# Kernel tuning notes

Measured on AMD Instinct MI355X. Metric: run time of the kernel, lower is better.

Reference implementation:

```python
import jax, jax.numpy as jnp
import numpy as np

E = 1024   # embed_dim
H = 16     # num_heads
DH = E // H
FF = 4096  # intermediate_size
EPS = 1e-5


def layernorm(x, g, b):
    mu = jnp.mean(x, axis=-1, keepdims=True)
    var = jnp.var(x, axis=-1, keepdims=True)
    return (x - mu) * jax.lax.rsqrt(var + EPS) * g + b


def setup_inputs() -> dict:
    key = jax.random.key(0)
    ks = jax.random.split(key, 16)
    s = 0.02
    return {
        "x": jax.random.normal(ks[0], (2, 2048, E), dtype=jnp.float32),
        "ln1_g": jnp.ones((E,), jnp.float32),
        "ln1_b": jnp.zeros((E,), jnp.float32),
        "ln2_g": jnp.ones((E,), jnp.float32),
        "ln2_b": jnp.zeros((E,), jnp.float32),
        # per-head Q/K/V projections stacked: [H, E, DH]
        "wq": jax.random.normal(ks[1], (H, E, DH), jnp.float32) * s,
        "bq": jnp.zeros((H, DH), jnp.float32),
        "wk": jax.random.normal(ks[2], (H, E, DH), jnp.float32) * s,
        "bk": jnp.zeros((H, DH), jnp.float32),
        "wv": jax.random.normal(ks[3], (H, E, DH), jnp.float32) * s,
        "bv": jnp.zeros((H, DH), jnp.float32),
        "wo": jax.random.normal(ks[4], (E, E), jnp.float32) * s,
        "bo": jnp.zeros((E,), jnp.float32),
        "w1": jax.random.normal(ks[5], (E, FF), jnp.float32) * s,
        "b1": jnp.zeros((FF,), jnp.float32),
        "w2": jax.random.normal(ks[6], (FF, E), jnp.float32) * s,
        "b2": jnp.zeros((E,), jnp.float32),
    }


def reference(x, ln1_g, ln1_b, ln2_g, ln2_b, wq, bq, wk, bk, wv, bv,
              wo, bo, w1, b1, w2, b2):
    # --- multi-head attention (pre-LN) ---
    h = layernorm(x, ln1_g, ln1_b)                       # [B,S,E]
    q = jnp.einsum('bse,hed->bhsd', h, wq) + bq[:, None, :]
    k = jnp.einsum('bse,hed->bhsd', h, wk) + bk[:, None, :]
    v = jnp.einsum('bse,hed->bhsd', h, wv) + bv[:, None, :]
    scores = jnp.einsum('bhsd,bhtd->bhst', q, k) / jnp.sqrt(
        jnp.asarray(DH, x.dtype))                        # [B,H,S,S]
    w = jax.nn.softmax(scores, axis=-1)
    attn = jnp.einsum('bhst,bhtd->bhsd', w, v)           # [B,H,S,DH]
    B, _, S, _ = attn.shape
    concat = attn.transpose(0, 2, 1, 3).reshape(B, S, E)  # head concat order
    x = x + concat @ wo + bo
    # --- feed-forward (pre-LN), exact GELU, dropout_p=0 ---
    h2 = layernorm(x, ln2_g, ln2_b)
    ff = jax.nn.gelu(h2 @ w1 + b1, approximate=False) @ w2 + b2
    return x + ff
```

## Files before the change

kernel.cpp:

```cpp
#include <hip/hip_runtime.h>
#include <hip/hip_bf16.h>
#include <math.h>

typedef __attribute__((ext_vector_type(8))) short short8;
typedef __attribute__((ext_vector_type(4))) float f32x4;
typedef __attribute__((ext_vector_type(16))) float f32x16;
typedef __attribute__((ext_vector_type(4))) unsigned u32x4;

#define MFMA_BF16(a, b, c) __builtin_amdgcn_mfma_f32_16x16x32_bf16(a, b, c, 0, 0, 0)
#define MFMA32_BF16(a, b, c) __builtin_amdgcn_mfma_f32_32x32x16_bf16(a, b, c, 0, 0, 0)

#define GLD_LDS16(g, l)                                              \
  __builtin_amdgcn_global_load_lds(                                  \
      (const __attribute__((address_space(1))) void*)(g),            \
      (__attribute__((address_space(3))) void*)(l), 16, 0, 0)

__device__ __forceinline__ unsigned cvt_pk_bf16(float lo, float hi) {
  unsigned r;
  asm("v_cvt_pk_bf16_f32 %0, %1, %2" : "=v"(r) : "v"(lo), "v"(hi));
  return r;
}
#define PSWAP(a, b) asm volatile("v_permlane32_swap_b32 %0, %1" : "+v"(a), "+v"(b))

__device__ __forceinline__ unsigned short f2bf(float f) {
  union { float f; unsigned u; } v; v.f = f;
  unsigned r = v.u + 0x7FFFu + ((v.u >> 16) & 1u);
  return (unsigned short)(r >> 16);
}
__device__ __forceinline__ float bf2f(unsigned short u) {
  union { unsigned u; float f; } v; v.u = ((unsigned)u) << 16;
  return v.f;
}

__global__ __launch_bounds__(256) void transpose_cast(
    const float* __restrict__ in, unsigned short* __restrict__ out,
    int R, int C, size_t in_bs, size_t out_bs) {
  __shared__ float t[32][33];
  const float* inp = in + blockIdx.z * in_bs;
  unsigned short* outp = out + blockIdx.z * out_bs;
  const int c0 = blockIdx.x * 32, r0 = blockIdx.y * 32;
  const int tx = threadIdx.x, ty = threadIdx.y;
#pragma unroll
  for (int i = 0; i < 32; i += 8)
    t[ty + i][tx] = inp[(size_t)(r0 + ty + i) * C + c0 + tx];
  __syncthreads();
#pragma unroll
  for (int i = 0; i < 32; i += 8)
    outp[(size_t)(c0 + ty + i) * R + r0 + tx] = f2bf(t[tx][ty + i]);
}

__global__ void concat_bias(const float* __restrict__ bq, const float* __restrict__ bk,
                            const float* __restrict__ bv, float* __restrict__ bcat) {
  int i = blockIdx.x * 256 + threadIdx.x;
  if (i < 1024) bcat[i] = bq[i];
  else if (i < 2048) bcat[i] = bk[i - 1024];
  else if (i < 3072) bcat[i] = bv[i - 2048];
}

__global__ __launch_bounds__(512) void vtrans(
    const unsigned short* __restrict__ qkv, unsigned short* __restrict__ vt) {
  __shared__ unsigned short t[64][65];
  const int bh = blockIdx.y;
  const int s0 = blockIdx.x * 64;
  const int tx = threadIdx.x;
  const int ty = threadIdx.y;
  const unsigned short* in =
      qkv + (size_t)(bh >> 4) * 2048 * 3072 + 2048 + (bh & 15) * 64;
#pragma unroll
  for (int i = 0; i < 8; ++i)
    t[ty * 8 + i][tx] = in[(size_t)(s0 + ty * 8 + i) * 3072 + tx];
  __syncthreads();
  unsigned short* o = vt + (size_t)bh * 64 * 2048 + s0;
#pragma unroll
  for (int i = 0; i < 8; ++i)
    o[(size_t)(ty * 8 + i) * 2048 + tx] = t[tx][ty * 8 + i];
}

__global__ __launch_bounds__(256) void ln_kernel(
    const float* __restrict__ x, const float* __restrict__ g,
    const float* __restrict__ bb, unsigned short* __restrict__ out) {
  const int row = blockIdx.x, tid = threadIdx.x;
  const float4 v = ((const float4*)(x + (size_t)row * 1024))[tid];
  float s = v.x + v.y + v.z + v.w;
  float ss = v.x * v.x + v.y * v.y + v.z * v.z + v.w * v.w;
#pragma unroll
  for (int k = 1; k < 64; k <<= 1) {
    s += __shfl_xor(s, k, 64);
    ss += __shfl_xor(ss, k, 64);
  }
  __shared__ float red[8];
  const int wid = tid >> 6;
  if ((tid & 63) == 0) { red[wid] = s; red[wid + 4] = ss; }
  __syncthreads();
  s = red[0] + red[1] + red[2] + red[3];
  ss = red[4] + red[5] + red[6] + red[7];
  const float mu = s * (1.0f / 1024.0f);
  const float var = ss * (1.0f / 1024.0f) - mu * mu;
  const float rs = rsqrtf(var + 1e-5f);
  const float4 gv = ((const float4*)g)[tid];
  const float4 bv = ((const float4*)bb)[tid];
  ushort4 o;
  o.x = f2bf((v.x - mu) * rs * gv.x + bv.x);
  o.y = f2bf((v.y - mu) * rs * gv.y + bv.y);
  o.z = f2bf((v.z - mu) * rs * gv.z + bv.z);
  o.w = f2bf((v.w - mu) * rs * gv.w + bv.w);
  ((ushort4*)(out + (size_t)row * 1024))[tid] = o;
}

template <int EPI, int BN>
__global__ __launch_bounds__(256, 3) void gemm_bt(
    const unsigned short* __restrict__ A, const unsigned short* __restrict__ Bt,
    const float* __restrict__ bias, const float* __restrict__ res,
    void* __restrict__ Cout, int M, int N, int K) {
  constexpr int NFR = BN / 32;
  constexpr int BISS = BN / 32;
  __shared__ unsigned short As[128 * 64];
  __shared__ unsigned short Bs[BN * 64];
  const int tid = threadIdx.x;
  const int wid = tid >> 6, lane = tid & 63;
  const int li = lane & 15, gi = lane >> 4;
  const int bm = blockIdx.y, bn = blockIdx.x;
  const int wr = (wid >> 1) << 6;
  const int wc = (wid & 1) * (BN / 2);

  f32x4 acc[4][NFR];
#pragma unroll
  for (int m = 0; m < 4; ++m)
#pragma unroll
    for (int n = 0; n < NFR; ++n) acc[m][n] = (f32x4)0.0f;

  const size_t Ksz = (size_t)K;
  const int srow = tid >> 3;
  const int segG = (tid & 7) ^ (srow & 7);
  const unsigned short* Ab = A + (size_t)(bm * 128 + srow) * Ksz + segG * 8;
  const unsigned short* Bb = Bt + (size_t)(bn * BN + srow) * Ksz + segG * 8;

  for (int kt = 0; kt < K; kt += 64) {
#pragma unroll
    for (int c = 0; c < 4; ++c)
      GLD_LDS16(Ab + (size_t)(c * 32) * Ksz + kt, As + c * 2048 + wid * 512);
#pragma unroll
    for (int c = 0; c < BISS; ++c)
      GLD_LDS16(Bb + (size_t)(c * 32) * Ksz + kt, Bs + c * 2048 + wid * 512);
    __syncthreads();
    short8 af[4][2], bf[NFR][2];
#pragma unroll
    for (int m = 0; m < 4; ++m)
#pragma unroll
      for (int kk = 0; kk < 2; ++kk) {
        const int row = wr + m * 16 + li;
        af[m][kk] = *(const short8*)(As + row * 64 + ((kk * 4 + gi) ^ (row & 7)) * 8);
      }
#pragma unroll
    for (int n = 0; n < NFR; ++n)
#pragma unroll
      for (int kk = 0; kk < 2; ++kk) {
        const int row = wc + n * 16 + li;
        bf[n][kk] = *(const short8*)(Bs + row * 64 + ((kk * 4 + gi) ^ (row & 7)) * 8);
      }
    __builtin_amdgcn_s_setprio(1);
#pragma unroll
    for (int m = 0; m < 4; ++m)
#pragma unroll
      for (int n = 0; n < NFR; ++n) {
        acc[m][n] = MFMA_BF16(af[m][0], bf[n][0], acc[m][n]);
        acc[m][n] = MFMA_BF16(af[m][1], bf[n][1], acc[m][n]);
      }
    __builtin_amdgcn_s_setprio(0);
    __syncthreads();
  }

  const int row_base = bm * 128 + wr + gi * 4;
  const int col_base = bn * BN + wc + li;
#pragma unroll
  for (int m = 0; m < 4; ++m) {
#pragma unroll
    for (int n = 0; n < NFR; ++n) {
      const int col = col_base + n * 16;
      const float bi = bias[col];
#pragma unroll
      for (int r = 0; r < 4; ++r) {
        const int row = row_base + m * 16 + r;
        float v = acc[m][n][r] + bi;
        if (EPI == 2) v = 0.5f * v * (1.0f + erff(v * 0.70710678118654752f));
        const size_t idx = (size_t)row * N + col;
        if (EPI == 1) ((float*)Cout)[idx] = v + res[idx];
        else ((unsigned short*)Cout)[idx] = f2bf(v);
      }
    }
  }
}

__global__ __launch_bounds__(256, 4) void attn_kernel(
    const unsigned short* __restrict__ qkv, const unsigned short* __restrict__ vt,
    unsigned short* __restrict__ op0, unsigned short* __restrict__ op1,
    float* __restrict__ lpart) {
  __shared__ unsigned short Kl[2][4096];
  const int tid = threadIdx.x;
  const int wid = tid >> 6, lane = tid & 63;
  const int l31 = lane & 31, hiq = lane >> 5;
  const int kvh = blockIdx.z & 1, b = blockIdx.z >> 1, h = blockIdx.y;
  const int q0 = blockIdx.x * 128 + wid * 32;
  const int LD = 3072;
  const size_t base = (size_t)b * 2048 * LD;
  const size_t kvoff = (size_t)kvh * 1024 * LD;

  short8 qb[4];
  {
    const unsigned short* qp = qkv + base + (size_t)(q0 + l31) * LD + h * 64 + hiq * 8;
#pragma unroll
    for (int ds = 0; ds < 4; ++ds) qb[ds] = *(const short8*)(qp + ds * 16);
  }

  f32x16 o0 = (f32x16)0.0f, o1 = (f32x16)0.0f;
  float la = 0.0f, lb = 0.0f;

  const int krw = lane >> 3;
  const int ksegG = (lane & 7) ^ krw;
  const unsigned short* kdma = qkv + base + kvoff + 1024 + h * 64 + ksegG * 8 +
                               (size_t)(wid * 16 + krw) * LD;

  const unsigned short* vbh =
      vt + (size_t)(b * 16 + h) * 64 * 2048 + kvh * 1024 + 8 * hiq;

  auto kstage = [&](int buf, int t) {
    GLD_LDS16(kdma + (size_t)t * 64 * LD, &Kl[buf][wid * 1024]);
    GLD_LDS16(kdma + (size_t)(t * 64 + 8) * LD, &Kl[buf][wid * 1024 + 512]);
  };

  kstage(0, 0);
  __syncthreads();

  for (int t = 0; t < 16; ++t) {
    if (t < 15) kstage((t + 1) & 1, t + 1);

    const unsigned short* kl = Kl[t & 1];
    short8 kf[2][4];
#pragma unroll
    for (int kvb = 0; kvb < 2; ++kvb)
#pragma unroll
      for (int ds = 0; ds < 4; ++ds)
        kf[kvb][ds] = *(const short8*)(
            kl + (kvb * 32 + l31) * 64 + (((2 * ds + hiq) ^ (l31 & 7)) * 8));

    f32x16 sA = (f32x16)0.0f, sB = (f32x16)0.0f;
    __builtin_amdgcn_s_setprio(1);
#pragma unroll
    for (int ds = 0; ds < 4; ++ds) {
      sA = MFMA32_BF16(kf[0][ds], qb[ds], sA);
      sB = MFMA32_BF16(kf[1][ds], qb[ds], sB);
    }
    __builtin_amdgcn_s_setprio(0);

    const unsigned short* vtt = vbh + 64 * t;
#pragma unroll
    for (int kvb = 0; kvb < 2; ++kvb) {
      const int ks0 = 2 * kvb;
      const short8 v00 = *(const short8*)(vtt + (size_t)l31 * 2048 + 16 * ks0);
      const short8 v01 = *(const short8*)(vtt + (size_t)l31 * 2048 + 16 * ks0 + 16);
      const short8 v10 = *(const short8*)(vtt + (size_t)(32 + l31) * 2048 + 16 * ks0);
      const short8 v11 = *(const short8*)(vtt + (size_t)(32 + l31) * 2048 + 16 * ks0 + 16);
      const f32x16 s = kvb ? sB : sA;
      unsigned P[8];
#pragma unroll
      for (int i = 0; i < 8; ++i) {
        const float pe = __expf(s[2 * i] * 0.125f);
        const float po = __expf(s[2 * i + 1] * 0.125f);
        la += pe; lb += po;
        P[i] = cvt_pk_bf16(pe, po);
      }
      PSWAP(P[0], P[2]); PSWAP(P[1], P[3]);
      PSWAP(P[4], P[6]); PSWAP(P[5], P[7]);
      const short8 pa0 = __builtin_bit_cast(short8, (u32x4){P[0], P[1], P[2], P[3]});
      const short8 pa1 = __builtin_bit_cast(short8, (u32x4){P[4], P[5], P[6], P[7]});
      __builtin_amdgcn_s_setprio(1);
      o0 = MFMA32_BF16(pa0, v00, o0);
      o0 = MFMA32_BF16(pa1, v01, o0);
      o1 = MFMA32_BF16(pa0, v10, o1);
      o1 = MFMA32_BF16(pa1, v11, o1);
      __builtin_amdgcn_s_setprio(0);
    }
    __syncthreads();
  }

  const float lsum = la + lb;
  const float lt = lsum + __shfl_xor(lsum, 32, 64);
  if (hiq == 0)
    lpart[(size_t)kvh * 65536 + ((size_t)(b * 2048 + q0 + l31) * 16) + h] = lt;

  unsigned short* op = kvh ? op1 : op0;
#pragma unroll
  for (int r = 0; r < 16; ++r) {
    const int crow = (r & 3) + 8 * (r >> 2) + 4 * hiq;
    const size_t rowb = (size_t)(b * 2048 + q0 + crow) * 1024 + h * 64 + l31;
    op[rowb]      = f2bf(o0[r]);
    op[rowb + 32] = f2bf(o1[r]);
  }
}

__global__ __launch_bounds__(256) void attn_combine(
    const unsigned short* __restrict__ op0, unsigned short* __restrict__ op1io,
    const float* __restrict__ lpart) {
  const size_t i8 = (size_t)blockIdx.x * 256 + threadIdx.x;
  const size_t g = (i8 * 8) >> 6;
  const float inv = 1.0f / (lpart[g] + lpart[g + 65536]);
  const short8 a = *(const short8*)(op0 + i8 * 8);
  const short8 c = *(const short8*)(op1io + i8 * 8);
  short8 o;
#pragma unroll
  for (int j = 0; j < 8; ++j)
    o[j] = (short)f2bf((bf2f((unsigned short)a[j]) + bf2f((unsigned short)c[j])) * inv);
  *(short8*)(op1io + i8 * 8) = o;
}

extern "C" void kernel_launch(void* const* d_in, const int* in_sizes, int n_in,
                              void* d_out, int out_size, void* d_ws, size_t ws_size,
                              hipStream_t stream) {
  const float* x     = (const float*)d_in[0];
  const float* ln1_g = (const float*)d_in[1];
  const float* ln1_b = (const float*)d_in[2];
  const float* ln2_g = (const float*)d_in[3];
  const float* ln2_b = (const float*)d_in[4];
  const float* wq    = (const float*)d_in[5];
  const float* bq    = (const float*)d_in[6];
  const float* wk    = (const float*)d_in[7];
  const float* bk    = (const float*)d_in[8];
  const float* wv    = (const float*)d_in[9];
  const float* bv    = (const float*)d_in[10];
  const float* wo    = (const float*)d_in[11];
  const float* bo    = (const float*)d_in[12];
  const float* w1    = (const float*)d_in[13];
  const float* b1    = (const float*)d_in[14];
  const float* w2    = (const float*)d_in[15];
  const float* b2    = (const float*)d_in[16];
  float* out = (float*)d_out;

  char* p = (char*)d_ws;
  unsigned short* ws_h     = (unsigned short*)p; p += 4096ull * 1024 * 2;
  unsigned short* ws_qkv   = (unsigned short*)p; p += 4096ull * 3072 * 2;
  unsigned short* ws_attn  = (unsigned short*)p; p += 4096ull * 1024 * 2;
  unsigned short* ws_wqkvT = (unsigned short*)p; p += 3072ull * 1024 * 2;
  unsigned short* ws_woT   = (unsigned short*)p; p += 1024ull * 1024 * 2;
  unsigned short* ws_w1T   = (unsigned short*)p; p += 4096ull * 1024 * 2;
  unsigned short* ws_w2T   = (unsigned short*)p; p += 1024ull * 4096 * 2;
  float*          ws_bqkv  = (float*)p;          p += 3072 * 4;
  float*          ws_l     = (float*)p;          p += 2ull * 65536 * 4;
  unsigned short* ws_ff = ws_qkv;
  unsigned short* ws_vt = ws_w1T;

  const dim3 tb(32, 8);
  transpose_cast<<<dim3(2, 32, 16), tb, 0, stream>>>(
      wq, ws_wqkvT, 1024, 64, (size_t)(1024 * 64), (size_t)(64 * 1024));
  transpose_cast<<<dim3(2, 32, 16), tb, 0, stream>>>(
      wk, ws_wqkvT + 1024ull * 1024, 1024, 64, (size_t)(1024 * 64), (size_t)(64 * 1024));
  transpose_cast<<<dim3(2, 32, 16), tb, 0, stream>>>(
      wv, ws_wqkvT + 2048ull * 1024, 1024, 64, (size_t)(1024 * 64), (size_t)(64 * 1024));
  transpose_cast<<<dim3(32, 32, 1), tb, 0, stream>>>(wo, ws_woT, 1024, 1024, 0, 0);
  concat_bias<<<12, 256, 0, stream>>>(bq, bk, bv, ws_bqkv);

  ln_kernel<<<4096, 256, 0, stream>>>(x, ln1_g, ln1_b, ws_h);
  gemm_bt<0, 128><<<dim3(24, 32), 256, 0, stream>>>(ws_h, ws_wqkvT, ws_bqkv, nullptr,
                                                    ws_qkv, 4096, 3072, 1024);
  vtrans<<<dim3(32, 32), dim3(64, 8), 0, stream>>>(ws_qkv, ws_vt);
  attn_kernel<<<dim3(16, 16, 4), 256, 0, stream>>>(ws_qkv, ws_vt, ws_h, ws_attn, ws_l);
  attn_combine<<<2048, 256, 0, stream>>>(ws_h, ws_attn, ws_l);
  transpose_cast<<<dim3(128, 32, 1), tb, 0, stream>>>(w1, ws_w1T, 1024, 4096, 0, 0);
  transpose_cast<<<dim3(32, 128, 1), tb, 0, stream>>>(w2, ws_w2T, 4096, 1024, 0, 0);
  gemm_bt<1, 64><<<dim3(16, 32), 256, 0, stream>>>(ws_attn, ws_woT, bo, x,
                                                   out, 4096, 1024, 1024);
  ln_kernel<<<4096, 256, 0, stream>>>(out, ln2_g, ln2_b, ws_h);
  gemm_bt<2, 128><<<dim3(32, 32), 256, 0, stream>>>(ws_h, ws_w1T, b1, nullptr,
                                                    ws_ff, 4096, 4096, 1024);
  gemm_bt<1, 64><<<dim3(16, 32), 256, 0, stream>>>(ws_ff, ws_w2T, b2, out,
                                                   out, 4096, 1024, 4096);
}
```

Baseline: 279.4 us.

## Double-buffer GEMM LDS tiles and stage V through LDS in attention

```diff
diff --git a/kernel.cpp b/kernel.cpp
--- a/kernel.cpp
+++ b/kernel.cpp
@@ -14,6 +14,14 @@
   __builtin_amdgcn_global_load_lds(                                  \
       (const __attribute__((address_space(1))) void*)(g),            \
       (__attribute__((address_space(3))) void*)(l), 16, 0, 0)
+
+template <int N>
+__device__ __forceinline__ void waitcnt_vm() {
+  if constexpr (N == 0) asm volatile("s_waitcnt vmcnt(0)" ::: "memory");
+  else if constexpr (N == 4) asm volatile("s_waitcnt vmcnt(4)" ::: "memory");
+  else if constexpr (N == 6) asm volatile("s_waitcnt vmcnt(6)" ::: "memory");
+  else if constexpr (N == 8) asm volatile("s_waitcnt vmcnt(8)" ::: "memory");
+}
 
 __device__ __forceinline__ unsigned cvt_pk_bf16(float lo, float hi) {
   unsigned r;
@@ -108,14 +116,15 @@
 }
 
 template <int EPI, int BN>
-__global__ __launch_bounds__(256, 3) void gemm_bt(
+__global__ __launch_bounds__(256, (BN == 128) ? 2 : 3) void gemm_bt(
     const unsigned short* __restrict__ A, const unsigned short* __restrict__ Bt,
     const float* __restrict__ bias, const float* __restrict__ res,
     void* __restrict__ Cout, int M, int N, int K) {
   constexpr int NFR = BN / 32;
   constexpr int BISS = BN / 32;
-  __shared__ unsigned short As[128 * 64];
-  __shared__ unsigned short Bs[BN * 64];
+  constexpr int ISS = 4 + BISS;
+  __shared__ unsigned short As[2][128 * 64];
+  __shared__ unsigned short Bs[2][BN * 64];
   const int tid = threadIdx.x;
   const int wid = tid >> 6, lane = tid & 63;
   const int li = lane & 15, gi = lane >> 4;
@@ -135,28 +144,32 @@
   const unsigned short* Ab = A + (size_t)(bm * 128 + srow) * Ksz + segG * 8;
   const unsigned short* Bb = Bt + (size_t)(bn * BN + srow) * Ksz + segG * 8;
 
-  for (int kt = 0; kt < K; kt += 64) {
+  auto stage = [&](int buf, int kt) {
 #pragma unroll
     for (int c = 0; c < 4; ++c)
-      GLD_LDS16(Ab + (size_t)(c * 32) * Ksz + kt, As + c * 2048 + wid * 512);
+      GLD_LDS16(Ab + (size_t)(c * 32) * Ksz + kt, &As[buf][c * 2048 + wid * 512]);
 #pragma unroll
     for (int c = 0; c < BISS; ++c)
-      GLD_LDS16(Bb + (size_t)(c * 32) * Ksz + kt, Bs + c * 2048 + wid * 512);
-    __syncthreads();
+      GLD_LDS16(Bb + (size_t)(c * 32) * Ksz + kt, &Bs[buf][c * 2048 + wid * 512]);
+  };
+
+  auto compute = [&](int ib) {
+    const unsigned short* As_ = As[ib];
+    const unsigned short* Bs_ = Bs[ib];
     short8 af[4][2], bf[NFR][2];
 #pragma unroll
     for (int m = 0; m < 4; ++m)
 #pragma unroll
       for (int kk = 0; kk < 2; ++kk) {
         const int row = wr + m * 16 + li;
-        af[m][kk] = *(const short8*)(As + row * 64 + ((kk * 4 + gi) ^ (row & 7)) * 8);
+        af[m][kk] = *(const short8*)(As_ + row * 64 + ((kk * 4 + gi) ^ (row & 7)) * 8);
       }
 #pragma unroll
     for (int n = 0; n < NFR; ++n)
 #pragma unroll
       for (int kk = 0; kk < 2; ++kk) {
         const int row = wc + n * 16 + li;
-        bf[n][kk] = *(const short8*)(Bs + row * 64 + ((kk * 4 + gi) ^ (row & 7)) * 8);
+        bf[n][kk] = *(const short8*)(Bs_ + row * 64 + ((kk * 4 + gi) ^ (row & 7)) * 8);
       }
     __builtin_amdgcn_s_setprio(1);
 #pragma unroll
@@ -167,8 +180,22 @@
         acc[m][n] = MFMA_BF16(af[m][1], bf[n][1], acc[m][n]);
       }
     __builtin_amdgcn_s_setprio(0);
-    __syncthreads();
-  }
+  };
+
+  const int KT = K >> 6;
+  stage(0, 0);
+  for (int i = 0; i < KT - 1; ++i) {
+    stage((i + 1) & 1, (i + 1) << 6);
+    waitcnt_vm<ISS>();
+    __builtin_amdgcn_s_barrier();
+    __builtin_amdgcn_sched_barrier(0);
+    compute(i & 1);
+    __builtin_amdgcn_s_barrier();
+  }
+  waitcnt_vm<0>();
+  __builtin_amdgcn_s_barrier();
+  __builtin_amdgcn_sched_barrier(0);
+  compute((KT - 1) & 1);
 
   const int row_base = bm * 128 + wr + gi * 4;
   const int col_base = bn * BN + wc + li;
@@ -196,6 +223,7 @@
     unsigned short* __restrict__ op0, unsigned short* __restrict__ op1,
     float* __restrict__ lpart) {
   __shared__ unsigned short Kl[2][4096];
+  __shared__ unsigned short Vl[2][4096];
   const int tid = threadIdx.x;
   const int wid = tid >> 6, lane = tid & 63;
   const int l31 = lane & 31, hiq = lane >> 5;
@@ -215,26 +243,25 @@
   f32x16 o0 = (f32x16)0.0f, o1 = (f32x16)0.0f;
   float la = 0.0f, lb = 0.0f;
 
-  const int krw = lane >> 3;
-  const int ksegG = (lane & 7) ^ krw;
-  const unsigned short* kdma = qkv + base + kvoff + 1024 + h * 64 + ksegG * 8 +
-                               (size_t)(wid * 16 + krw) * LD;
-
-  const unsigned short* vbh =
-      vt + (size_t)(b * 16 + h) * 64 * 2048 + kvh * 1024 + 8 * hiq;
+  const int rw = lane >> 3;
+  const int sgG = (lane & 7) ^ rw;
+  const unsigned short* kdma = qkv + base + kvoff + 1024 + h * 64 + sgG * 8 +
+                               (size_t)(wid * 16 + rw) * LD;
+  const unsigned short* vdma = vt + (size_t)(b * 16 + h) * 64 * 2048 +
+                               (size_t)(wid * 16 + rw) * 2048 + kvh * 1024 + sgG * 8;
 
   auto kstage = [&](int buf, int t) {
     GLD_LDS16(kdma + (size_t)t * 64 * LD, &Kl[buf][wid * 1024]);
     GLD_LDS16(kdma + (size_t)(t * 64 + 8) * LD, &Kl[buf][wid * 1024 + 512]);
   };
-
-  kstage(0, 0);
-  __syncthreads();
-
-  for (int t = 0; t < 16; ++t) {
-    if (t < 15) kstage((t + 1) & 1, t + 1);
-
-    const unsigned short* kl = Kl[t & 1];
+  auto vstage = [&](int buf, int t) {
+    GLD_LDS16(vdma + t * 64, &Vl[buf][wid * 1024]);
+    GLD_LDS16(vdma + 8 * 2048 + t * 64, &Vl[buf][wid * 1024 + 512]);
+  };
+
+  auto compute = [&](int ib) {
+    const unsigned short* kl = Kl[ib];
+    const unsigned short* vl = Vl[ib];
     short8 kf[2][4];
 #pragma unroll
     for (int kvb = 0; kvb < 2; ++kvb)
@@ -252,14 +279,8 @@
     }
     __builtin_amdgcn_s_setprio(0);
 
-    const unsigned short* vtt = vbh + 64 * t;
 #pragma unroll
     for (int kvb = 0; kvb < 2; ++kvb) {
-      const int ks0 = 2 * kvb;
-      const short8 v00 = *(const short8*)(vtt + (size_t)l31 * 2048 + 16 * ks0);
-      const short8 v01 = *(const short8*)(vtt + (size_t)l31 * 2048 + 16 * ks0 + 16);
-      const short8 v10 = *(const short8*)(vtt + (size_t)(32 + l31) * 2048 + 16 * ks0);
-      const short8 v11 = *(const short8*)(vtt + (size_t)(32 + l31) * 2048 + 16 * ks0 + 16);
       const f32x16 s = kvb ? sB : sA;
       unsigned P[8];
 #pragma unroll
@@ -273,6 +294,11 @@
       PSWAP(P[4], P[6]); PSWAP(P[5], P[7]);
       const short8 pa0 = __builtin_bit_cast(short8, (u32x4){P[0], P[1], P[2], P[3]});
       const short8 pa1 = __builtin_bit_cast(short8, (u32x4){P[4], P[5], P[6], P[7]});
+      const int sg0 = 4 * kvb + hiq, sg1 = 4 * kvb + 2 + hiq;
+      const short8 v00 = *(const short8*)(vl + l31 * 64 + ((sg0 ^ (l31 & 7)) * 8));
+      const short8 v01 = *(const short8*)(vl + l31 * 64 + ((sg1 ^ (l31 & 7)) * 8));
+      const short8 v10 = *(const short8*)(vl + (32 + l31) * 64 + ((sg0 ^ (l31 & 7)) * 8));
+      const short8 v11 = *(const short8*)(vl + (32 + l31) * 64 + ((sg1 ^ (l31 & 7)) * 8));
       __builtin_amdgcn_s_setprio(1);
       o0 = MFMA32_BF16(pa0, v00, o0);
       o0 = MFMA32_BF16(pa1, v01, o0);
@@ -280,8 +306,23 @@
       o1 = MFMA32_BF16(pa1, v11, o1);
       __builtin_amdgcn_s_setprio(0);
     }
-    __syncthreads();
-  }
+  };
+
+  kstage(0, 0);
+  vstage(0, 0);
+  for (int t = 0; t < 15; ++t) {
+    kstage((t + 1) & 1, t + 1);
+    vstage((t + 1) & 1, t + 1);
+    waitcnt_vm<4>();
+    __builtin_amdgcn_s_barrier();
+    __builtin_amdgcn_sched_barrier(0);
+    compute(t & 1);
+    __builtin_amdgcn_s_barrier();
+  }
+  waitcnt_vm<0>();
+  __builtin_amdgcn_s_barrier();
+  __builtin_amdgcn_sched_barrier(0);
+  compute(15 & 1);
 
   const float lsum = la + lb;
   const float lt = lsum + __shfl_xor(lsum, 32, 64);
```

Result: faster. 264.3 us (-5.4%).
